# Optimization experiments

Hardware: AMD Instinct MI355X
Metric: run time of the kernel (lower is better)

The kernel has to match this reference:

```python
import jax, jax.numpy as jnp
import numpy as np

D_MODEL = 1024
NUM_HEADS = 16
D_K = D_MODEL // NUM_HEADS


def setup_inputs() -> dict:
    key = jax.random.key(0)
    ks = jax.random.split(key, 9)
    B, S = 2, 2048
    s = 1.0 / np.sqrt(D_MODEL)
    inp = {
        "x": jax.random.normal(ks[0], (B, S, D_MODEL), dtype=jnp.float32),
        "Wq": jax.random.normal(ks[1], (D_MODEL, D_MODEL), dtype=jnp.float32) * s,
        "bq": jnp.zeros((D_MODEL,), dtype=jnp.float32),
        "Wk": jax.random.normal(ks[2], (D_MODEL, D_MODEL), dtype=jnp.float32) * s,
        "bk": jnp.zeros((D_MODEL,), dtype=jnp.float32),
        "Wv": jax.random.normal(ks[3], (D_MODEL, D_MODEL), dtype=jnp.float32) * s,
        "bv": jnp.zeros((D_MODEL,), dtype=jnp.float32),
        "Wo": jax.random.normal(ks[4], (D_MODEL, D_MODEL), dtype=jnp.float32) * s,
        "bo": jnpp if False else jnp.zeros((D_MODEL,), dtype=jnp.float32),
    }
    return inp


def reference(x, Wq, bq, Wk, bk, Wv, bv, Wo, bo):
    B, S, _ = x.shape
    H, Dk = NUM_HEADS, D_K

    def proj(W, b):
        # [B,S,D] -> [B,H,S,Dk]
        return (x @ W + b).reshape(B, S, H, Dk).transpose(0, 2, 1, 3)

    Q = proj(Wq, bq)
    K = proj(Wk, bk)
    V = proj(Wv, bv)

    scores = jnp.einsum("bhqd,bhkd->bhqk", Q, K) / np.sqrt(Dk)
    attn = jax.nn.softmax(scores, axis=-1)  # no mask, dropout p=0 (eval)
    out = jnp.einsum("bhqk,bhkd->bhqd", attn, V)
    out = out.transpose(0, 2, 1, 3).reshape(B, S, D_MODEL)
    return out @ Wo + bo
```

## Files before the change

### kernel.cpp

```cpp
#include <hip/hip_runtime.h>
#include <hip/hip_bf16.h>
#include <cstdint>
#include <math.h>

#define D_MODEL 1024
#define NHEADS  16
#define DK      64
#define BATCH   2
#define SEQ     2048
#define M_TOTAL (BATCH*SEQ)
#define NSPLIT  2
#define NTS     (SEQ/64/NSPLIT)

using f32x4  = __attribute__((ext_vector_type(4)))  float;
using f32x16 = __attribute__((ext_vector_type(16))) float;
using s16x8  = __attribute__((ext_vector_type(8)))  short;

#define CSC (0.125f * 1.44269504088896341f)

__device__ __forceinline__ unsigned short bf16r(float f) {
    __hip_bfloat16 h = __float2bfloat16(f);
    return *(unsigned short*)&h;
}
__device__ __forceinline__ uint32_t cvtpk(float lo, float hi) {
    uint32_t r;
    asm("v_cvt_pk_bf16_f32 %0, %1, %2" : "=v"(r) : "v"(lo), "v"(hi));
    return r;
}
__device__ __forceinline__ float b2f(unsigned short u) {
    uint32_t x = (uint32_t)u << 16;
    float f;
    __builtin_memcpy(&f, &x, 4);
    return f;
}

__global__ __launch_bounds__(256) void conv_x(const float* __restrict__ x,
                                              unsigned short* __restrict__ xb)
{
    const size_t i = ((size_t)blockIdx.x * 256 + threadIdx.x) * 8;
    const float4 a = *(const float4*)(x + i);
    const float4 b = *(const float4*)(x + i + 4);
    ushort4 r0, r1;
    r0.x = bf16r(a.x); r0.y = bf16r(a.y); r0.z = bf16r(a.z); r0.w = bf16r(a.w);
    r1.x = bf16r(b.x); r1.y = bf16r(b.y); r1.z = bf16r(b.z); r1.w = bf16r(b.w);
    *(ushort4*)(xb + i)     = r0;
    *(ushort4*)(xb + i + 4) = r1;
}

__global__ __launch_bounds__(256) void conv_wt(const float* __restrict__ W0, const float* __restrict__ W1,
                                               const float* __restrict__ W2, const float* __restrict__ W3,
                                               unsigned short* __restrict__ T0, unsigned short* __restrict__ T1,
                                               unsigned short* __restrict__ T2, unsigned short* __restrict__ T3)
{
    const float* W; unsigned short* T;
    switch (blockIdx.z) {
        case 0: W = W0; T = T0; break;
        case 1: W = W1; T = T1; break;
        case 2: W = W2; T = T2; break;
        default: W = W3; T = T3; break;
    }
    __shared__ float tile[32][33];
    const int t  = threadIdx.x;
    const int r  = t >> 3;
    const int c4 = (t & 7) * 4;
    const int k0 = blockIdx.x * 32;
    const int n0 = blockIdx.y * 32;

    const float4 v = *(const float4*)(W + (size_t)(k0 + r) * 1024 + n0 + c4);
    tile[r][c4 + 0] = v.x; tile[r][c4 + 1] = v.y; tile[r][c4 + 2] = v.z; tile[r][c4 + 3] = v.w;
    __syncthreads();
    ushort4 o;
    o.x = bf16r(tile[c4 + 0][r]);
    o.y = bf16r(tile[c4 + 1][r]);
    o.z = bf16r(tile[c4 + 2][r]);
    o.w = bf16r(tile[c4 + 3][r]);
    *(ushort4*)(T + (size_t)(n0 + r) * 1024 + k0 + c4) = o;
}

template<int OUT_BF16>
__device__ __forceinline__ void gemm_mfma_body(const unsigned short* __restrict__ A,
                                               const unsigned short* __restrict__ Bt,
                                               const float* __restrict__ bias,
                                               void* __restrict__ C,
                                               float oscale)
{
    __shared__ unsigned short As[128 * 64];
    __shared__ unsigned short Bs[128 * 64];

    const int t    = threadIdx.x;
    const int w    = t >> 6;
    const int lane = t & 63;
    const int ln   = lane & 15;
    const int g    = lane >> 4;
    const int wr   = w >> 1, wc = w & 1;
    const int m0   = blockIdx.y * 128;
    const int n0   = blockIdx.x * 128;

    f32x4 acc[4][4];
#pragma unroll
    for (int mi = 0; mi < 4; ++mi)
#pragma unroll
        for (int ni = 0; ni < 4; ++ni)
#pragma unroll
            for (int j = 0; j < 4; ++j) acc[mi][ni][j] = 0.f;

    const int lrow = lane >> 3;
    const int lchk = (lane & 7) ^ lrow;
    const unsigned short* Ag = A  + (size_t)(m0 + w * 32 + lrow) * 1024 + lchk * 8;
    const unsigned short* Bg = Bt + (size_t)(n0 + w * 32 + lrow) * 1024 + lchk * 8;

    for (int kt = 0; kt < 16; ++kt) {
        const int k0 = kt * 64;
#pragma unroll
        for (int i = 0; i < 4; ++i) {
            __builtin_amdgcn_global_load_lds(Ag + (size_t)i * 8 * 1024 + k0,
                                             &As[(w * 32 + i * 8) * 64], 16, 0, 0);
            __builtin_amdgcn_global_load_lds(Bg + (size_t)i * 8 * 1024 + k0,
                                             &Bs[(w * 32 + i * 8) * 64], 16, 0, 0);
        }
        __syncthreads();

#pragma unroll
        for (int ks = 0; ks < 2; ++ks) {
            s16x8 af[4], bf[4];
#pragma unroll
            for (int mi = 0; mi < 4; ++mi) {
                const int row = wr * 64 + mi * 16 + ln;
                af[mi] = *(const s16x8*)((const char*)As + row * 128 +
                                         (((ks * 4 + g) ^ (ln & 7)) * 16));
            }
#pragma unroll
            for (int ni = 0; ni < 4; ++ni) {
                const int row = wc * 64 + ni * 16 + ln;
                bf[ni] = *(const s16x8*)((const char*)Bs + row * 128 +
                                         (((ks * 4 + g) ^ (ln & 7)) * 16));
            }
#pragma unroll
            for (int mi = 0; mi < 4; ++mi)
#pragma unroll
                for (int ni = 0; ni < 4; ++ni)
                    acc[mi][ni] = __builtin_amdgcn_mfma_f32_16x16x32_bf16(
                        af[mi], bf[ni], acc[mi][ni], 0, 0, 0);
        }
        __syncthreads();
    }

#pragma unroll
    for (int ni = 0; ni < 4; ++ni) {
        const int n = n0 + wc * 64 + ni * 16 + ln;
        const float bn = bias[n];
#pragma unroll
        for (int mi = 0; mi < 4; ++mi) {
            const int m = m0 + wr * 64 + mi * 16 + g * 4;
#pragma unroll
            for (int j = 0; j < 4; ++j) {
                const float v = (acc[mi][ni][j] + bn) * oscale;
                if constexpr (OUT_BF16)
                    ((unsigned short*)C)[(size_t)(m + j) * 1024 + n] = bf16r(v);
                else
                    ((float*)C)[(size_t)(m + j) * 1024 + n] = v;
            }
        }
    }
}

__global__ __launch_bounds__(256) void qkv_mfma(const unsigned short* __restrict__ xb,
                                                const unsigned short* __restrict__ Wqt, const float* __restrict__ bq,
                                                const unsigned short* __restrict__ Wkt, const float* __restrict__ bk,
                                                const unsigned short* __restrict__ Wvt, const float* __restrict__ bv,
                                                unsigned short* __restrict__ Q,
                                                unsigned short* __restrict__ K,
                                                unsigned short* __restrict__ V)
{
    if (blockIdx.z == 0)      gemm_mfma_body<1>(xb, Wqt, bq, Q, CSC);
    else if (blockIdx.z == 1) gemm_mfma_body<1>(xb, Wkt, bk, K, 1.0f);
    else                      gemm_mfma_body<1>(xb, Wvt, bv, V, 1.0f);
}

__global__ __launch_bounds__(256) void oproj_mfma(const unsigned short* __restrict__ Ab,
                                                  const unsigned short* __restrict__ Wot,
                                                  const float* __restrict__ bo,
                                                  float* __restrict__ C)
{
    gemm_mfma_body<0>(Ab, Wot, bo, C, 1.0f);
}

__global__ __launch_bounds__(256) void attn_mfma(const unsigned short* __restrict__ Qb,
                                                 const unsigned short* __restrict__ Kb,
                                                 const unsigned short* __restrict__ Vb,
                                                 unsigned short* __restrict__ Opart,
                                                 float2* __restrict__ ml)
{
    __shared__ unsigned short Klds [2][64 * 64];
    __shared__ unsigned short Vtlds[2][64 * 64];

    const int t   = threadIdx.x;
    const int wid = t >> 6;
    const int l   = t & 63;
    const int q32 = l & 31;
    const int hi  = l >> 5;

    const int bh = blockIdx.y;
    const int b  = bh >> 4;
    const int h  = bh & 15;
    const int sp = blockIdx.z;
    const int qbase = blockIdx.x * 128 + wid * 32;
    const size_t qrow = (size_t)(b * SEQ + qbase + q32);
    const size_t kv0  = (size_t)(b * SEQ) + (size_t)sp * (SEQ / NSPLIT);

    s16x8 qf[4];
    {
        const unsigned short* qp = Qb + qrow * D_MODEL + h * DK + 8 * hi;
#pragma unroll
        for (int ks = 0; ks < 4; ++ks) qf[ks] = *(const s16x8*)(qp + 16 * ks);
    }

    f32x16 ot0, ot1;
#pragma unroll
    for (int i = 0; i < 16; ++i) { ot0[i] = 0.f; ot1[i] = 0.f; }
    float lsum = 0.f;

    const int skey = t >> 3;
    const int sc8  = t & 7;
    const int vk2  = 2 * (t & 31);
    const int vd0  = 8 * (t >> 5);
    const unsigned short* Kg = Kb + (kv0 + skey) * D_MODEL + h * DK + 8 * sc8;
    const unsigned short* Vg = Vb + (kv0 + vk2) * D_MODEL + h * DK + vd0;
    const int kwo0 = skey * 128        + 16 * (sc8 ^ (skey & 7));
    const int kwo1 = (skey + 32) * 128 + 16 * (sc8 ^ (skey & 7));

    s16x8 kr0, kr1, vr0, vr1;

    auto load_regs = [&](int kt) {
        const size_t off = (size_t)kt * 64 * D_MODEL;
        kr0 = *(const s16x8*)(Kg + off);
        kr1 = *(const s16x8*)(Kg + off + (size_t)32 * D_MODEL);
        vr0 = *(const s16x8*)(Vg + off);
        vr1 = *(const s16x8*)(Vg + off + D_MODEL);
    };
    auto write_stage = [&](int buf) {
        *(s16x8*)((char*)&Klds[buf][0] + kwo0) = kr0;
        *(s16x8*)((char*)&Klds[buf][0] + kwo1) = kr1;
#pragma unroll
        for (int i = 0; i < 8; ++i) {
            const int d = vd0 + i;
            const uint32_t val = (uint32_t)(unsigned short)vr0[i] |
                                 ((uint32_t)(unsigned short)vr1[i] << 16);
            *(uint32_t*)((char*)&Vtlds[buf][0] + d * 128 +
                         16 * ((vk2 >> 3) ^ (d & 7)) + (vk2 & 7) * 2) = val;
        }
    };

    load_regs(0);
    write_stage(0);
    load_regs(1);
    __syncthreads();

    for (int kt = 0; kt < NTS; ++kt) {
        const int cur = kt & 1;
        if (kt + 1 < NTS) write_stage(cur ^ 1);
        if (kt + 2 < NTS) load_regs(kt + 2);

        const char* Kl = (const char*)&Klds[cur][0];
        const char* Vl = (const char*)&Vtlds[cur][0];

        f32x16 s0, s1;
#pragma unroll
        for (int i = 0; i < 16; ++i) { s0[i] = 0.f; s1[i] = 0.f; }
        __builtin_amdgcn_s_setprio(1);
#pragma unroll
        for (int ks = 0; ks < 4; ++ks) {
            const int c = hi + 2 * ks;
            const s16x8 a0 = *(const s16x8*)(Kl + q32 * 128 + 16 * (c ^ (q32 & 7)));
            const s16x8 a1 = *(const s16x8*)(Kl + (q32 + 32) * 128 + 16 * (c ^ (q32 & 7)));
            s0 = __builtin_amdgcn_mfma_f32_32x32x16_bf16(a0, qf[ks], s0, 0, 0, 0);
            s1 = __builtin_amdgcn_mfma_f32_32x32x16_bf16(a1, qf[ks], s1, 0, 0, 0);
        }
        __builtin_amdgcn_s_setprio(0);

        float la = 0.f, lb = 0.f, lc = 0.f, ld = 0.f;
#pragma unroll
        for (int i = 0; i < 4; ++i) {
            s0[4 * i + 0] = exp2f(s0[4 * i + 0]); la += s0[4 * i + 0];
            s0[4 * i + 1] = exp2f(s0[4 * i + 1]); lb += s0[4 * i + 1];
            s0[4 * i + 2] = exp2f(s0[4 * i + 2]); lc += s0[4 * i + 2];
            s0[4 * i + 3] = exp2f(s0[4 * i + 3]); ld += s0[4 * i + 3];
            s1[4 * i + 0] = exp2f(s1[4 * i + 0]); la += s1[4 * i + 0];
            s1[4 * i + 1] = exp2f(s1[4 * i + 1]); lb += s1[4 * i + 1];
            s1[4 * i + 2] = exp2f(s1[4 * i + 2]); lc += s1[4 * i + 2];
            s1[4 * i + 3] = exp2f(s1[4 * i + 3]); ld += s1[4 * i + 3];
        }
        lsum += (la + lb) + (lc + ld);

        s16x8 pf[4];
#pragma unroll
        for (int half = 0; half < 2; ++half) {
            const f32x16& sv = half ? s1 : s0;
            uint32_t W[8], Y[8];
#pragma unroll
            for (int j = 0; j < 8; ++j) W[j] = cvtpk(sv[2 * j], sv[2 * j + 1]);
#pragma unroll
            for (int j = 0; j < 8; ++j) Y[j] = __shfl_xor(W[j], 32);
            union { uint32_t u[4]; s16x8 v; } F0, F1;
            F0.u[0] = hi ? Y[2] : W[0];
            F0.u[1] = hi ? Y[3] : W[1];
            F0.u[2] = hi ? W[2] : Y[0];
            F0.u[3] = hi ? W[3] : Y[1];
            F1.u[0] = hi ? Y[6] : W[4];
            F1.u[1] = hi ? Y[7] : W[5];
            F1.u[2] = hi ? W[6] : Y[4];
            F1.u[3] = hi ? W[7] : Y[5];
            pf[2 * half]     = F0.v;
            pf[2 * half + 1] = F1.v;
        }

        __builtin_amdgcn_s_setprio(1);
#pragma unroll
        for (int ks = 0; ks < 4; ++ks) {
            const int c = hi + 2 * ks;
            const s16x8 av0 = *(const s16x8*)(Vl + q32 * 128 + 16 * (c ^ (q32 & 7)));
            const s16x8 av1 = *(const s16x8*)(Vl + (q32 + 32) * 128 + 16 * (c ^ (q32 & 7)));
            ot0 = __builtin_amdgcn_mfma_f32_32x32x16_bf16(av0, pf[ks], ot0, 0, 0, 0);
            ot1 = __builtin_amdgcn_mfma_f32_32x32x16_bf16(av1, pf[ks], ot1, 0, 0, 0);
        }
        __builtin_amdgcn_s_setprio(0);

        __syncthreads();
    }

    const float ltot = lsum + __shfl_xor(lsum, 32);
    const size_t prow = (size_t)bh * SEQ + qbase + q32;
    if (hi == 0)
        ml[(size_t)sp * (BATCH * NHEADS * SEQ) + prow] = make_float2(0.f, ltot);

    unsigned short* op = Opart + (size_t)sp * ((size_t)BATCH * NHEADS * SEQ * DK)
                               + prow * DK;
#pragma unroll
    for (int j = 0; j < 4; ++j) {
        uint2 st0, st1;
        st0.x = cvtpk(ot0[4 * j + 0], ot0[4 * j + 1]);
        st0.y = cvtpk(ot0[4 * j + 2], ot0[4 * j + 3]);
        st1.x = cvtpk(ot1[4 * j + 0], ot1[4 * j + 1]);
        st1.y = cvtpk(ot1[4 * j + 2], ot1[4 * j + 3]);
        *(uint2*)(op + 8 * j + 4 * hi)      = st0;
        *(uint2*)(op + 32 + 8 * j + 4 * hi) = st1;
    }
}

__global__ __launch_bounds__(256) void attn_combine(const unsigned short* __restrict__ Opart,
                                                    const float2* __restrict__ ml,
                                                    unsigned short* __restrict__ Ab)
{
    const int tid = blockIdx.x * 256 + threadIdx.x;
    const int row = tid >> 3;
    const int d0  = (tid & 7) * 8;
    const size_t NROW = (size_t)BATCH * NHEADS * SEQ;

    const float2 a = ml[row];
    const float2 c = ml[NROW + row];
    const float mm = fmaxf(a.x, c.x);
    const float w0 = exp2f(a.x - mm);
    const float w1 = exp2f(c.x - mm);
    const float rinv = 1.0f / (w0 * a.y + w1 * c.y);

    const size_t src = (size_t)row * DK + d0;
    const ushort4 u0 = *(const ushort4*)(Opart + src);
    const ushort4 u1 = *(const ushort4*)(Opart + src + 4);
    const ushort4 v0 = *(const ushort4*)(Opart + NROW * DK + src);
    const ushort4 v1 = *(const ushort4*)(Opart + NROW * DK + src + 4);

    const int bh = row >> 11, s = row & 2047;
    const int b = bh >> 4, h = bh & 15;
    unsigned short* dst = Ab + ((size_t)(b * SEQ + s)) * D_MODEL + h * DK + d0;

    ushort4 o0, o1;
    o0.x = bf16r((w0 * b2f(u0.x) + w1 * b2f(v0.x)) * rinv);
    o0.y = bf16r((w0 * b2f(u0.y) + w1 * b2f(v0.y)) * rinv);
    o0.z = bf16r((w0 * b2f(u0.z) + w1 * b2f(v0.z)) * rinv);
    o0.w = bf16r((w0 * b2f(u0.w) + w1 * b2f(v0.w)) * rinv);
    o1.x = bf16r((w0 * b2f(u1.x) + w1 * b2f(v1.x)) * rinv);
    o1.y = bf16r((w0 * b2f(u1.y) + w1 * b2f(v1.y)) * rinv);
    o1.z = bf16r((w0 * b2f(u1.z) + w1 * b2f(v1.z)) * rinv);
    o1.w = bf16r((w0 * b2f(u1.w) + w1 * b2f(v1.w)) * rinv);
    *(ushort4*)(dst)     = o0;
    *(ushort4*)(dst + 4) = o1;
}

extern "C" void kernel_launch(void* const* d_in, const int* in_sizes, int n_in,
                              void* d_out, int out_size, void* d_ws, size_t ws_size,
                              hipStream_t stream)
{
    const float* x  = (const float*)d_in[0];
    const float* Wq = (const float*)d_in[1];
    const float* bq = (const float*)d_in[2];
    const float* Wk = (const float*)d_in[3];
    const float* bk = (const float*)d_in[4];
    const float* Wv = (const float*)d_in[5];
    const float* bv = (const float*)d_in[6];
    const float* Wo = (const float*)d_in[7];
    const float* bo = (const float*)d_in[8];

    float* out = (float*)d_out;

    const size_t mat  = (size_t)M_TOTAL * D_MODEL;
    const size_t wmat = (size_t)D_MODEL * D_MODEL;
    unsigned short* xb  = (unsigned short*)d_ws;
    unsigned short* Wqt = xb  + mat;
    unsigned short* Wkt = Wqt + wmat;
    unsigned short* Wvt = Wkt + wmat;
    unsigned short* Wot = Wvt + wmat;
    unsigned short* Qb  = Wot + wmat;
    unsigned short* Kb  = Qb  + mat;
    unsigned short* Vb  = Kb  + mat;
    unsigned short* Ab  = Vb  + mat;
    unsigned short* Op  = Ab  + mat;
    float2*         ml  = (float2*)d_ws;

    conv_x<<<dim3(2048), 256, 0, stream>>>(x, xb);
    conv_wt<<<dim3(32, 32, 4), 256, 0, stream>>>(Wq, Wk, Wv, Wo, Wqt, Wkt, Wvt, Wot);

    qkv_mfma<<<dim3(8, 32, 3), 256, 0, stream>>>(xb, Wqt, bq, Wkt, bk, Wvt, bv, Qb, Kb, Vb);

    attn_mfma<<<dim3(SEQ / 128, BATCH * NHEADS, NSPLIT), 256, 0, stream>>>(Qb, Kb, Vb, Op, ml);

    attn_combine<<<dim3((BATCH * NHEADS * SEQ * 8) / 256), 256, 0, stream>>>(Op, ml, Ab);

    oproj_mfma<<<dim3(8, 32), 256, 0, stream>>>(Ab, Wot, bo, out);
}
```

Before: 157.1 us.

## Permute V^T key order to drop P shuffles and single-buffer LDS

The V^T tile in LDS is now written with a permuted key order (bits 2 and 3 of the key index swapped), so the exponentiated score accumulators can be packed straight into PV MFMA operands. This removes the eight cross-lane shuffles and selects per half-tile. LDS is cut from double to single buffering, with an extra barrier before each stage write, and __launch_bounds__(256,4) asks for higher occupancy. The risk is an additional sync per tile and less load/compute overlap in exchange for fewer VALU/DPP ops and lower LDS and register use.

```diff
diff --git a/kernel.cpp b/kernel.cpp
--- a/kernel.cpp
+++ b/kernel.cpp
@@ -185,14 +185,14 @@
     gemm_mfma_body<0>(Ab, Wot, bo, C, 1.0f);
 }
 
-__global__ __launch_bounds__(256) void attn_mfma(const unsigned short* __restrict__ Qb,
-                                                 const unsigned short* __restrict__ Kb,
-                                                 const unsigned short* __restrict__ Vb,
-                                                 unsigned short* __restrict__ Opart,
-                                                 float2* __restrict__ ml)
-{
-    __shared__ unsigned short Klds [2][64 * 64];
-    __shared__ unsigned short Vtlds[2][64 * 64];
+__global__ __launch_bounds__(256, 4) void attn_mfma(const unsigned short* __restrict__ Qb,
+                                                    const unsigned short* __restrict__ Kb,
+                                                    const unsigned short* __restrict__ Vb,
+                                                    unsigned short* __restrict__ Opart,
+                                                    float2* __restrict__ ml)
+{
+    __shared__ unsigned short Klds [64 * 64];
+    __shared__ unsigned short Vtlds[64 * 64];
 
     const int t   = threadIdx.x;
     const int wid = t >> 6;
@@ -223,11 +223,12 @@
     const int skey = t >> 3;
     const int sc8  = t & 7;
     const int vk2  = 2 * (t & 31);
+    const int pk2  = (vk2 & ~12) | ((vk2 & 4) << 1) | ((vk2 & 8) >> 1);
     const int vd0  = 8 * (t >> 5);
     const unsigned short* Kg = Kb + (kv0 + skey) * D_MODEL + h * DK + 8 * sc8;
     const unsigned short* Vg = Vb + (kv0 + vk2) * D_MODEL + h * DK + vd0;
-    const int kwo0 = skey * 128        + 16 * (sc8 ^ (skey & 7));
-    const int kwo1 = (skey + 32) * 128 + 16 * (sc8 ^ (skey & 7));
+    char* const kw0 = (char*)Klds + skey * 128        + 16 * (sc8 ^ (skey & 7));
+    char* const kw1 = (char*)Klds + (skey + 32) * 128 + 16 * (sc8 ^ (skey & 7));
 
     s16x8 kr0, kr1, vr0, vr1;
 
@@ -238,31 +239,25 @@
         vr0 = *(const s16x8*)(Vg + off);
         vr1 = *(const s16x8*)(Vg + off + D_MODEL);
     };
-    auto write_stage = [&](int buf) {
-        *(s16x8*)((char*)&Klds[buf][0] + kwo0) = kr0;
-        *(s16x8*)((char*)&Klds[buf][0] + kwo1) = kr1;
+    auto write_stage = [&]() {
+        *(s16x8*)kw0 = kr0;
+        *(s16x8*)kw1 = kr1;
 #pragma unroll
         for (int i = 0; i < 8; ++i) {
             const int d = vd0 + i;
             const uint32_t val = (uint32_t)(unsigned short)vr0[i] |
                                  ((uint32_t)(unsigned short)vr1[i] << 16);
-            *(uint32_t*)((char*)&Vtlds[buf][0] + d * 128 +
-                         16 * ((vk2 >> 3) ^ (d & 7)) + (vk2 & 7) * 2) = val;
+            *(uint32_t*)((char*)Vtlds + d * 128 +
+                         16 * ((pk2 >> 3) ^ (d & 7)) + (pk2 & 7) * 2) = val;
         }
     };
 
     load_regs(0);
-    write_stage(0);
-    load_regs(1);
+    write_stage();
     __syncthreads();
 
     for (int kt = 0; kt < NTS; ++kt) {
-        const int cur = kt & 1;
-        if (kt + 1 < NTS) write_stage(cur ^ 1);
-        if (kt + 2 < NTS) load_regs(kt + 2);
-
-        const char* Kl = (const char*)&Klds[cur][0];
-        const char* Vl = (const char*)&Vtlds[cur][0];
+        if (kt < NTS - 1) load_regs(kt + 1);
 
         f32x16 s0, s1;
 #pragma unroll
@@ -271,8 +266,8 @@
 #pragma unroll
         for (int ks = 0; ks < 4; ++ks) {
             const int c = hi + 2 * ks;
-            const s16x8 a0 = *(const s16x8*)(Kl + q32 * 128 + 16 * (c ^ (q32 & 7)));
-            const s16x8 a1 = *(const s16x8*)(Kl + (q32 + 32) * 128 + 16 * (c ^ (q32 & 7)));
+            const s16x8 a0 = *(const s16x8*)((char*)Klds + q32 * 128 + 16 * (c ^ (q32 & 7)));
+            const s16x8 a1 = *(const s16x8*)((char*)Klds + (q32 + 32) * 128 + 16 * (c ^ (q32 & 7)));
             s0 = __builtin_amdgcn_mfma_f32_32x32x16_bf16(a0, qf[ks], s0, 0, 0, 0);
             s1 = __builtin_amdgcn_mfma_f32_32x32x16_bf16(a1, qf[ks], s1, 0, 0, 0);
         }
@@ -293,38 +288,35 @@
         lsum += (la + lb) + (lc + ld);
 
         s16x8 pf[4];
-#pragma unroll
-        for (int half = 0; half < 2; ++half) {
-            const f32x16& sv = half ? s1 : s0;
-            uint32_t W[8], Y[8];
-#pragma unroll
-            for (int j = 0; j < 8; ++j) W[j] = cvtpk(sv[2 * j], sv[2 * j + 1]);
-#pragma unroll
-            for (int j = 0; j < 8; ++j) Y[j] = __shfl_xor(W[j], 32);
-            union { uint32_t u[4]; s16x8 v; } F0, F1;
-            F0.u[0] = hi ? Y[2] : W[0];
-            F0.u[1] = hi ? Y[3] : W[1];
-            F0.u[2] = hi ? W[2] : Y[0];
-            F0.u[3] = hi ? W[3] : Y[1];
-            F1.u[0] = hi ? Y[6] : W[4];
-            F1.u[1] = hi ? Y[7] : W[5];
-            F1.u[2] = hi ? W[6] : Y[4];
-            F1.u[3] = hi ? W[7] : Y[5];
-            pf[2 * half]     = F0.v;
-            pf[2 * half + 1] = F1.v;
+        {
+            union { uint32_t u[4]; s16x8 v; } F;
+#pragma unroll
+            for (int e = 0; e < 4; ++e) F.u[e] = cvtpk(s0[2 * e], s0[2 * e + 1]);
+            pf[0] = F.v;
+#pragma unroll
+            for (int e = 0; e < 4; ++e) F.u[e] = cvtpk(s0[8 + 2 * e], s0[9 + 2 * e]);
+            pf[1] = F.v;
+#pragma unroll
+            for (int e = 0; e < 4; ++e) F.u[e] = cvtpk(s1[2 * e], s1[2 * e + 1]);
+            pf[2] = F.v;
+#pragma unroll
+            for (int e = 0; e < 4; ++e) F.u[e] = cvtpk(s1[8 + 2 * e], s1[9 + 2 * e]);
+            pf[3] = F.v;
         }
 
         __builtin_amdgcn_s_setprio(1);
 #pragma unroll
         for (int ks = 0; ks < 4; ++ks) {
             const int c = hi + 2 * ks;
-            const s16x8 av0 = *(const s16x8*)(Vl + q32 * 128 + 16 * (c ^ (q32 & 7)));
-            const s16x8 av1 = *(const s16x8*)(Vl + (q32 + 32) * 128 + 16 * (c ^ (q32 & 7)));
+            const s16x8 av0 = *(const s16x8*)((char*)Vtlds + q32 * 128 + 16 * (c ^ (q32 & 7)));
+            const s16x8 av1 = *(const s16x8*)((char*)Vtlds + (q32 + 32) * 128 + 16 * (c ^ (q32 & 7)));
             ot0 = __builtin_amdgcn_mfma_f32_32x32x16_bf16(av0, pf[ks], ot0, 0, 0, 0);
             ot1 = __builtin_amdgcn_mfma_f32_32x32x16_bf16(av1, pf[ks], ot1, 0, 0, 0);
         }
         __builtin_amdgcn_s_setprio(0);
 
+        __syncthreads();
+        if (kt < NTS - 1) write_stage();
         __syncthreads();
     }
 
```

After: 142.7 us. 1.1x faster.
